# Kernel tuning notes

Measured on AMD Instinct MI355X. Metric: run time of the kernel, lower is better.

## Reference

```python
import jax, jax.numpy as jnp
import numpy as np

T, B, P, H = 4096, 16, 512, 512
DT_MIN, DT_MAX = 1e-3, 0.1


def setup_inputs() -> dict:
    key = jax.random.key(0)
    k_in, k_b, k_dt = jax.random.split(key, 3)
    inputs = jax.random.normal(k_in, (T, B, H), dtype=jnp.float32)
    # HiPPO-diag init: a_diag = -sqrt(2n+1)*sqrt(2n+3); log_neg_a = log(-a_diag)
    n = jnp.arange(P, dtype=jnp.float32)
    log_neg_a = jnp.log(jnp.sqrt(2 * n + 1) * jnp.sqrt(2 * n + 3))
    b = jax.random.normal(k_b, (P, H), dtype=jnp.float32) * 0.01
    log_dt = jax.random.uniform(k_dt, (P,), dtype=jnp.float32) * (
        np.float32(np.log(DT_MAX)) - np.float32(np.log(DT_MIN))
    ) + np.float32(np.log(DT_MIN))
    return {"inputs": inputs, "log_neg_a": log_neg_a, "b": b, "log_dt": log_dt}


def reference(inputs, log_neg_a, b, log_dt):
    # Discretization (matches torch module exactly, including extra dt factor)
    dt = jnp.exp(log_dt)                       # [P]
    a = -jnp.exp(log_neg_a)                    # [P]
    a_bar = jnp.exp(dt * a)                    # [P]
    b_bar = ((a_bar - 1.0) / a)[:, None] * b * dt[:, None]  # [P, H]

    # Precompute driving term for all timesteps: u_t @ b_bar.T -> [T, B, P]
    bu = jnp.einsum("tbh,ph->tbp", inputs, b_bar)

    batch = inputs.shape[1]
    z0 = jnp.zeros((batch, a_bar.shape[0]), dtype=inputs.dtype)

    def step(z, bu_t):
        z = a_bar[None, :] * z + bu_t
        return z, z

    _, zs = jax.lax.scan(step, z0, bu)  # [T, B, P]
    return zs
```

## Files before the change

### kernel.cpp

```cpp
#include <hip/hip_runtime.h>
#include <math.h>

#define T_DIM 4096
#define B_DIM 16
#define P_DIM 512
#define H_DIM 512
#define M_DIM (T_DIM * B_DIM)
#define BP (B_DIM * P_DIM)
#define BP4 (BP / 4)
#define P4 (P_DIM / 4)

#define KBYTES (H_DIM * 2)
#define BK 64

#define CLEN_F 8
#define CHUNKS_F (T_DIM / CLEN_F)
#define GROUP 16
#define NGROUPS (CHUNKS_F / GROUP)
#define CLEN_S 64
#define CHUNKS_S (T_DIM / CLEN_S)

#define SCALE_B 1048576.0f
#define INV_SCALE_B (1.0f / 1048576.0f)

typedef _Float16 f16x8 __attribute__((ext_vector_type(8)));
typedef float f32x4 __attribute__((ext_vector_type(4)));

__device__ __forceinline__ void gload16(const void* g, void* l) {
    __builtin_amdgcn_global_load_lds(
        (const __attribute__((address_space(1))) void*)(uintptr_t)g,
        (__attribute__((address_space(3))) void*)(uint32_t)(uintptr_t)l,
        16, 0, 0);
}

__global__ __launch_bounds__(256) void precompute_kernel(
    const float* __restrict__ log_neg_a,
    const float* __restrict__ b,
    const float* __restrict__ log_dt,
    float* __restrict__ b_bar,
    _Float16* __restrict__ b_bar16,
    float* __restrict__ a_bar,
    float* __restrict__ aL8,
    float* __restrict__ aL128,
    float* __restrict__ aL64,
    float* __restrict__ aL8pow,
    int write16) {
    int idx = blockIdx.x * blockDim.x + threadIdx.x;
    if (idx >= P_DIM * H_DIM) return;
    int p = idx >> 9;
    float dt = expf(log_dt[p]);
    float a  = -expf(log_neg_a[p]);
    float x  = dt * a;
    float scale = (expm1f(x) / a) * dt;
    float bb = scale * b[idx];
    b_bar[idx] = bb;
    if (write16) b_bar16[idx] = (_Float16)(bb * SCALE_B);
    if ((idx & (H_DIM - 1)) == 0) {
        a_bar[p] = expf(x);
        float l8 = expf(x * 8.0f);
        aL8[p]   = l8;
        aL128[p] = expf(x * 128.0f);
        aL64[p]  = expf(x * 64.0f);
        float pw = 1.0f;
        for (int j = 0; j < GROUP; ++j) {
            aL8pow[j * P_DIM + p] = pw;
            pw *= l8;
        }
    }
}

__global__ __launch_bounds__(256) void convert_a_kernel(
    const float4* __restrict__ in, f16x8* __restrict__ out) {
    int t = blockIdx.x * blockDim.x + threadIdx.x;
    float4 v0 = in[(size_t)t * 2];
    float4 v1 = in[(size_t)t * 2 + 1];
    f16x8 o;
    o[0] = (_Float16)v0.x; o[1] = (_Float16)v0.y;
    o[2] = (_Float16)v0.z; o[3] = (_Float16)v0.w;
    o[4] = (_Float16)v1.x; o[5] = (_Float16)v1.y;
    o[6] = (_Float16)v1.z; o[7] = (_Float16)v1.w;
    out[t] = o;
}

__global__ __launch_bounds__(256) void gemm16_scan_kernel(
    const char* __restrict__ A16,
    const char* __restrict__ B16,
    const float* __restrict__ a_bar,
    float* __restrict__ Cout,
    float* __restrict__ carry) {
    __shared__ char As[128 * BK * 2];
    __shared__ char Bs[128 * BK * 2];

    const int tid  = threadIdx.x;
    const int lane = tid & 63;
    const int wid  = tid >> 6;
    const int rowBase = blockIdx.y * 128;
    const int colBase = blockIdx.x * 128;

    const int srow = tid >> 3;
    const int scol = ((tid & 7) << 4) ^ ((srow & 7) << 4);
    const char* gA = A16 + (size_t)(rowBase + srow) * KBYTES + scol;
    const char* gB = B16 + (size_t)(colBase + srow) * KBYTES + scol;

    f32x4 acc[4][4];
#pragma unroll
    for (int m2 = 0; m2 < 4; ++m2)
#pragma unroll
        for (int n2 = 0; n2 < 4; ++n2)
            acc[m2][n2] = (f32x4){0.f, 0.f, 0.f, 0.f};

    const int wr = wid >> 1;
    const int wc = wid & 1;

    for (int kt = 0; kt < H_DIM / BK; ++kt) {
#pragma unroll
        for (int i = 0; i < 4; ++i) {
            gload16(gA + (size_t)i * 32 * KBYTES, As + (i * 256 + wid * 64) * 16);
            gload16(gB + (size_t)i * 32 * KBYTES, Bs + (i * 256 + wid * 64) * 16);
        }
        gA += BK * 2;
        gB += BK * 2;
        __syncthreads();

#pragma unroll
        for (int kk = 0; kk < 2; ++kk) {
            const int kbyte = kk * 64 + ((lane >> 4) << 4);
            f16x8 af[4], bf[4];
#pragma unroll
            for (int m2 = 0; m2 < 4; ++m2) {
                int row = wr * 64 + m2 * 16 + (lane & 15);
                af[m2] = *(const f16x8*)(As + row * 128 + (kbyte ^ ((row & 7) << 4)));
            }
#pragma unroll
            for (int n2 = 0; n2 < 4; ++n2) {
                int col = wc * 64 + n2 * 16 + (lane & 15);
                bf[n2] = *(const f16x8*)(Bs + col * 128 + (kbyte ^ ((col & 7) << 4)));
            }
#pragma unroll
            for (int m2 = 0; m2 < 4; ++m2)
#pragma unroll
                for (int n2 = 0; n2 < 4; ++n2)
                    acc[m2][n2] = __builtin_amdgcn_mfma_f32_16x16x32_f16(
                        af[m2], bf[n2], acc[m2][n2], 0, 0, 0);
        }
        __syncthreads();
    }

    float* lds_z = (float*)As;
    const int pl = wc * 64 + (lane & 15);

    float ab[4];
#pragma unroll
    for (int n2 = 0; n2 < 4; ++n2) ab[n2] = a_bar[colBase + pl + n2 * 16];

    if (wr == 0) {
#pragma unroll
        for (int n2 = 0; n2 < 4; ++n2)
#pragma unroll
            for (int r = 0; r < 4; ++r) {
                float z = 0.f;
#pragma unroll
                for (int m2 = 0; m2 < 4; ++m2) {
                    z = fmaf(ab[n2], z, acc[m2][n2][r]);
                    acc[m2][n2][r] = z;
                }
                lds_z[((lane >> 4) * 4 + r) * 128 + pl + n2 * 16] = z;
            }
    }
    __syncthreads();
    if (wr == 1) {
#pragma unroll
        for (int n2 = 0; n2 < 4; ++n2)
#pragma unroll
            for (int r = 0; r < 4; ++r) {
                float z = lds_z[((lane >> 4) * 4 + r) * 128 + pl + n2 * 16];
#pragma unroll
                for (int m2 = 0; m2 < 4; ++m2) {
                    z = fmaf(ab[n2], z, acc[m2][n2][r]);
                    acc[m2][n2][r] = z;
                }
                int b = (lane >> 4) * 4 + r;
                carry[(size_t)blockIdx.y * BP + b * P_DIM + colBase + pl + n2 * 16] =
                    z * INV_SCALE_B;
            }
    }

#pragma unroll
    for (int m2 = 0; m2 < 4; ++m2) {
#pragma unroll
        for (int r = 0; r < 4; ++r) {
            size_t row = (size_t)(rowBase + wr * 64 + m2 * 16 + (lane >> 4) * 4 + r);
            float* po = Cout + row * P_DIM + colBase + wc * 64 + (lane & 15);
#pragma unroll
            for (int n2 = 0; n2 < 4; ++n2)
                po[n2 * 16] = acc[m2][n2][r] * INV_SCALE_B;
        }
    }
}

__global__ __launch_bounds__(256) void group_scan_kernel(
    const float4* __restrict__ carry,
    const float4* __restrict__ aL8_4,
    float4* __restrict__ y,
    float4* __restrict__ G) {
    int tid = blockIdx.x * blockDim.x + threadIdx.x;
    int bp4 = tid & (BP4 - 1);
    int g = tid >> 11;
    float4 ab = aL8_4[bp4 & (P4 - 1)];
    float4 z = make_float4(0.f, 0.f, 0.f, 0.f);
#pragma unroll
    for (int j = 0; j < GROUP; ++j) {
        size_t c = (size_t)(g * GROUP + j) * BP4 + bp4;
        y[c] = z;
        float4 v = carry[c];
        z.x = fmaf(ab.x, z.x, v.x);
        z.y = fmaf(ab.y, z.y, v.y);
        z.z = fmaf(ab.z, z.z, v.z);
        z.w = fmaf(ab.w, z.w, v.w);
    }
    G[(size_t)g * BP4 + bp4] = z;
}

__global__ __launch_bounds__(256) void gcarry_scan_kernel(
    const float* __restrict__ G,
    const float* __restrict__ aL128,
    float* __restrict__ gz) {
    int bp = blockIdx.x * blockDim.x + threadIdx.x;
    float aL = aL128[bp & (P_DIM - 1)];
    float z = 0.f;
#pragma unroll
    for (int g = 0; g < NGROUPS; ++g) {
        gz[g * BP + bp] = z;
        z = fmaf(aL, z, G[g * BP + bp]);
    }
}

__global__ __launch_bounds__(256) void fixup8_kernel(
    float4* __restrict__ zio,
    const float4* __restrict__ a_bar4,
    const float4* __restrict__ y,
    const float4* __restrict__ gz,
    const float4* __restrict__ aL8pow4) {
    int tid = blockIdx.x * blockDim.x + threadIdx.x;
    int bp4 = tid & (BP4 - 1);
    int c = (tid >> 11) + 1;
    int p4 = bp4 & (P4 - 1);
    int g = c >> 4;
    int j = c & (GROUP - 1);
    float4 ab = a_bar4[p4];
    float4 pw = aL8pow4[j * P4 + p4];
    float4 yy = y[(size_t)c * BP4 + bp4];
    float4 gzz = gz[(size_t)g * BP4 + bp4];
    float4 zin;
    zin.x = fmaf(pw.x, gzz.x, yy.x);
    zin.y = fmaf(pw.y, gzz.y, yy.y);
    zin.z = fmaf(pw.z, gzz.z, yy.z);
    zin.w = fmaf(pw.w, gzz.w, yy.w);
    float4 f = ab;
    size_t base = (size_t)c * CLEN_F * BP4 + bp4;
#pragma unroll
    for (int i = 0; i < CLEN_F; ++i) {
        size_t off = base + (size_t)i * BP4;
        float4 v = zio[off];
        v.x = fmaf(f.x, zin.x, v.x);
        v.y = fmaf(f.y, zin.y, v.y);
        v.z = fmaf(f.z, zin.z, v.z);
        v.w = fmaf(f.w, zin.w, v.w);
        zio[off] = v;
        f.x *= ab.x;
        f.y *= ab.y;
        f.z *= ab.z;
        f.w *= ab.w;
    }
}

#define BM 128
#define BN 128
#define BKF 16
__global__ __launch_bounds__(256) void gemm_kernel(
    const float* __restrict__ A,
    const float* __restrict__ Bm,
    float* __restrict__ Cout) {
    __shared__ float As[BM][BKF + 1];
    __shared__ float Bs[BN][BKF + 4];
    const int K = H_DIM;
    const int N = P_DIM;
    int tid = threadIdx.x;
    int tx = tid & 15;
    int ty = tid >> 4;
    int rowBase = blockIdx.y * BM;
    int colBase = blockIdx.x * BN;
    float acc[8][8];
#pragma unroll
    for (int i = 0; i < 8; ++i)
#pragma unroll
        for (int j = 0; j < 8; ++j) acc[i][j] = 0.f;
    for (int kt = 0; kt < K; kt += BKF) {
#pragma unroll
        for (int l = 0; l < 2; ++l) {
            int fl = tid * 2 + l;
            int row = fl >> 2;
            int kq = fl & 3;
            float4 av = *reinterpret_cast<const float4*>(
                &A[(size_t)(rowBase + row) * K + kt + kq * 4]);
            As[row][kq * 4 + 0] = av.x;
            As[row][kq * 4 + 1] = av.y;
            As[row][kq * 4 + 2] = av.z;
            As[row][kq * 4 + 3] = av.w;
            float4 bv = *reinterpret_cast<const float4*>(
                &Bm[(size_t)(colBase + row) * K + kt + kq * 4]);
            *reinterpret_cast<float4*>(&Bs[row][kq * 4]) = bv;
        }
        __syncthreads();
#pragma unroll
        for (int k = 0; k < BKF; ++k) {
            float af[8], bf[8];
#pragma unroll
            for (int i = 0; i < 8; ++i) af[i] = As[ty * 8 + i][k];
#pragma unroll
            for (int j = 0; j < 8; ++j) bf[j] = Bs[tx + 16 * j][k];
#pragma unroll
            for (int i = 0; i < 8; ++i)
#pragma unroll
                for (int j = 0; j < 8; ++j)
                    acc[i][j] = fmaf(af[i], bf[j], acc[i][j]);
        }
        __syncthreads();
    }
#pragma unroll
    for (int i = 0; i < 8; ++i) {
        size_t r = (size_t)(rowBase + ty * 8 + i);
#pragma unroll
        for (int j = 0; j < 8; ++j)
            Cout[r * N + colBase + tx + 16 * j] = acc[i][j];
    }
}

__global__ __launch_bounds__(256) void scan_local_kernel(
    float4* __restrict__ zio,
    const float4* __restrict__ a_bar4,
    float4* __restrict__ carry) {
    int tid = blockIdx.x * blockDim.x + threadIdx.x;
    int bp4 = tid & (BP4 - 1);
    int c = tid >> 11;
    float4 ab = a_bar4[bp4 & (P4 - 1)];
    size_t base = (size_t)c * CLEN_S * BP4 + bp4;
    float4 z = make_float4(0.f, 0.f, 0.f, 0.f);
    for (int i = 0; i < CLEN_S; ++i) {
        size_t off = base + (size_t)i * BP4;
        float4 v = zio[off];
        z.x = fmaf(ab.x, z.x, v.x);
        z.y = fmaf(ab.y, z.y, v.y);
        z.z = fmaf(ab.z, z.z, v.z);
        z.w = fmaf(ab.w, z.w, v.w);
        zio[off] = z;
    }
    carry[tid] = z;
}

__global__ __launch_bounds__(256) void carry_scan_kernel(
    const float4* __restrict__ carry,
    const float4* __restrict__ aL4,
    float4* __restrict__ z_in,
    int nchunks) {
    int bp4 = blockIdx.x * blockDim.x + threadIdx.x;
    float4 aL = aL4[bp4 & (P4 - 1)];
    float4 z = make_float4(0.f, 0.f, 0.f, 0.f);
    for (int c = 0; c < nchunks; ++c) {
        z_in[(size_t)c * BP4 + bp4] = z;
        float4 v = carry[(size_t)c * BP4 + bp4];
        z.x = fmaf(aL.x, z.x, v.x);
        z.y = fmaf(aL.y, z.y, v.y);
        z.z = fmaf(aL.z, z.z, v.z);
        z.w = fmaf(aL.w, z.w, v.w);
    }
}

__global__ __launch_bounds__(256) void fixup_kernel(
    float4* __restrict__ zio,
    const float4* __restrict__ a_bar4,
    const float4* __restrict__ z_in,
    int clen) {
    int tid = blockIdx.x * blockDim.x + threadIdx.x;
    int bp4 = tid & (BP4 - 1);
    int c = (tid >> 11) + 1;
    float4 ab = a_bar4[bp4 & (P4 - 1)];
    float4 zin = z_in[(size_t)c * BP4 + bp4];
    float4 f = ab;
    size_t base = (size_t)c * clen * BP4 + bp4;
    for (int i = 0; i < clen; ++i) {
        size_t off = base + (size_t)i * BP4;
        float4 v = zio[off];
        v.x = fmaf(f.x, zin.x, v.x);
        v.y = fmaf(f.y, zin.y, v.y);
        v.z = fmaf(f.z, zin.z, v.z);
        v.w = fmaf(f.w, zin.w, v.w);
        zio[off] = v;
        f.x *= ab.x;
        f.y *= ab.y;
        f.z *= ab.z;
        f.w *= ab.w;
    }
}

extern "C" void kernel_launch(void* const* d_in, const int* in_sizes, int n_in,
                              void* d_out, int out_size, void* d_ws, size_t ws_size,
                              hipStream_t stream) {
    const float* inputs    = (const float*)d_in[0];
    const float* log_neg_a = (const float*)d_in[1];
    const float* b         = (const float*)d_in[2];
    const float* log_dt    = (const float*)d_in[3];
    float* out = (float*)d_out;
    float* ws  = (float*)d_ws;

    float* b_bar   = ws;
    float* a_bar   = b_bar + P_DIM * H_DIM;
    float* aL8     = a_bar + P_DIM;
    float* aL128   = aL8 + P_DIM;
    float* aL64    = aL128 + P_DIM;
    float* aL8pow  = aL64 + P_DIM;
    float* carry   = aL8pow + GROUP * P_DIM;
    float* y       = carry + (size_t)CHUNKS_F * BP;
    float* G       = y + (size_t)CHUNKS_F * BP;
    float* gz      = G + (size_t)NGROUPS * BP;
    float* tail    = gz + (size_t)NGROUPS * BP;
    _Float16* b_bar16 = (_Float16*)tail;
    _Float16* A16     = b_bar16 + P_DIM * H_DIM;

    size_t ws_need = (size_t)((char*)(A16 + (size_t)M_DIM * H_DIM) - (char*)ws);
    int fast = (ws_size >= ws_need);

    precompute_kernel<<<(P_DIM * H_DIM) / 256, 256, 0, stream>>>(
        log_neg_a, b, log_dt, b_bar, b_bar16, a_bar, aL8, aL128, aL64, aL8pow, fast);

    if (fast) {
        convert_a_kernel<<<(M_DIM * H_DIM / 8) / 256, 256, 0, stream>>>(
            (const float4*)inputs, (f16x8*)A16);

        dim3 ggrid(P_DIM / 128, M_DIM / 128);
        gemm16_scan_kernel<<<ggrid, 256, 0, stream>>>(
            (const char*)A16, (const char*)b_bar16, a_bar, out, carry);

        group_scan_kernel<<<(NGROUPS * BP4) / 256, 256, 0, stream>>>(
            (const float4*)carry, (const float4*)aL8, (float4*)y, (float4*)G);

        gcarry_scan_kernel<<<BP / 256, 256, 0, stream>>>(G, aL128, gz);

        fixup8_kernel<<<((CHUNKS_F - 1) * BP4) / 256, 256, 0, stream>>>(
            (float4*)out, (const float4*)a_bar, (const float4*)y,
            (const float4*)gz, (const float4*)aL8pow);
    } else {
        dim3 ggrid(P_DIM / BN, M_DIM / BM);
        gemm_kernel<<<ggrid, 256, 0, stream>>>(inputs, b_bar, out);

        scan_local_kernel<<<(CHUNKS_S * BP4) / 256, 256, 0, stream>>>(
            (float4*)out, (const float4*)a_bar, (float4*)carry);

        carry_scan_kernel<<<BP4 / 256, 256, 0, stream>>>(
            (const float4*)carry, (const float4*)aL64, (float4*)y, CHUNKS_S);

        fixup_kernel<<<((CHUNKS_S - 1) * BP4) / 256, 256, 0, stream>>>(
            (float4*)out, (const float4*)a_bar, (const float4*)y, CLEN_S);
    }
}
```

Measured before the change: 161.3 us.

## Fuse fp32-to-fp16 input conversion into GEMM tile load

Removes the separate kernel that converted the fp32 inputs into an fp16 copy in workspace. The GEMM now loads fp32 A tiles straight into LDS with a swizzled layout and converts them to fp16 in registers before the MFMA. This avoids writing the 64 MB fp16 copy and reading it back. In exchange each GEMM block reads twice as many A bytes from global memory (the A input is read once per P-tile, of which there are four), uses double the LDS for A, and spends extra conversion instructions inside the inner loop.

```diff
diff --git a/kernel.cpp b/kernel.cpp
--- a/kernel.cpp
+++ b/kernel.cpp
@@ -10,7 +10,6 @@
 #define BP4 (BP / 4)
 #define P4 (P_DIM / 4)
 
-#define KBYTES (H_DIM * 2)
 #define BK 64
 
 #define CLEN_F 8
@@ -69,26 +68,13 @@
     }
 }
 
-__global__ __launch_bounds__(256) void convert_a_kernel(
-    const float4* __restrict__ in, f16x8* __restrict__ out) {
-    int t = blockIdx.x * blockDim.x + threadIdx.x;
-    float4 v0 = in[(size_t)t * 2];
-    float4 v1 = in[(size_t)t * 2 + 1];
-    f16x8 o;
-    o[0] = (_Float16)v0.x; o[1] = (_Float16)v0.y;
-    o[2] = (_Float16)v0.z; o[3] = (_Float16)v0.w;
-    o[4] = (_Float16)v1.x; o[5] = (_Float16)v1.y;
-    o[6] = (_Float16)v1.z; o[7] = (_Float16)v1.w;
-    out[t] = o;
-}
-
-__global__ __launch_bounds__(256) void gemm16_scan_kernel(
-    const char* __restrict__ A16,
+__global__ __launch_bounds__(256) void gemm_f32a_scan_kernel(
+    const float* __restrict__ A,
     const char* __restrict__ B16,
     const float* __restrict__ a_bar,
     float* __restrict__ Cout,
     float* __restrict__ carry) {
-    __shared__ char As[128 * BK * 2];
+    __shared__ char As[128 * BK * 4];
     __shared__ char Bs[128 * BK * 2];
 
     const int tid  = threadIdx.x;
@@ -97,10 +83,13 @@
     const int rowBase = blockIdx.y * 128;
     const int colBase = blockIdx.x * 128;
 
+    const int arow = tid >> 4;
+    const int acolb = (((tid & 15) ^ ((tid >> 4) & 7)) << 4);
+    const char* gA = (const char*)(A + (size_t)(rowBase + arow) * H_DIM) + acolb;
+
     const int srow = tid >> 3;
-    const int scol = ((tid & 7) << 4) ^ ((srow & 7) << 4);
-    const char* gA = A16 + (size_t)(rowBase + srow) * KBYTES + scol;
-    const char* gB = B16 + (size_t)(colBase + srow) * KBYTES + scol;
+    const int scolb = ((tid & 7) << 4) ^ ((srow & 7) << 4);
+    const char* gB = B16 + (size_t)(colBase + srow) * (H_DIM * 2) + scolb;
 
     f32x4 acc[4][4];
 #pragma unroll
@@ -114,27 +103,37 @@
 
     for (int kt = 0; kt < H_DIM / BK; ++kt) {
 #pragma unroll
-        for (int i = 0; i < 4; ++i) {
-            gload16(gA + (size_t)i * 32 * KBYTES, As + (i * 256 + wid * 64) * 16);
-            gload16(gB + (size_t)i * 32 * KBYTES, Bs + (i * 256 + wid * 64) * 16);
-        }
-        gA += BK * 2;
+        for (int i = 0; i < 8; ++i)
+            gload16(gA + (size_t)i * 16 * (H_DIM * 4), As + (i * 256 + wid * 64) * 16);
+#pragma unroll
+        for (int i = 0; i < 4; ++i)
+            gload16(gB + (size_t)i * 32 * (H_DIM * 2), Bs + (i * 256 + wid * 64) * 16);
+        gA += BK * 4;
         gB += BK * 2;
         __syncthreads();
 
 #pragma unroll
         for (int kk = 0; kk < 2; ++kk) {
-            const int kbyte = kk * 64 + ((lane >> 4) << 4);
+            const int ch0 = kk * 8 + ((lane >> 4) << 1);
+            const int kbyteB = kk * 64 + ((lane >> 4) << 4);
             f16x8 af[4], bf[4];
 #pragma unroll
             for (int m2 = 0; m2 < 4; ++m2) {
                 int row = wr * 64 + m2 * 16 + (lane & 15);
-                af[m2] = *(const f16x8*)(As + row * 128 + (kbyte ^ ((row & 7) << 4)));
+                int sw = (row & 7);
+                float4 a0 = *(const float4*)(As + row * 256 + ((ch0 ^ sw) << 4));
+                float4 a1 = *(const float4*)(As + row * 256 + (((ch0 + 1) ^ sw) << 4));
+                f16x8 v;
+                v[0] = (_Float16)a0.x; v[1] = (_Float16)a0.y;
+                v[2] = (_Float16)a0.z; v[3] = (_Float16)a0.w;
+                v[4] = (_Float16)a1.x; v[5] = (_Float16)a1.y;
+                v[6] = (_Float16)a1.z; v[7] = (_Float16)a1.w;
+                af[m2] = v;
             }
 #pragma unroll
             for (int n2 = 0; n2 < 4; ++n2) {
                 int col = wc * 64 + n2 * 16 + (lane & 15);
-                bf[n2] = *(const f16x8*)(Bs + col * 128 + (kbyte ^ ((col & 7) << 4)));
+                bf[n2] = *(const f16x8*)(Bs + col * 128 + (kbyteB ^ ((col & 7) << 4)));
             }
 #pragma unroll
             for (int m2 = 0; m2 < 4; ++m2)
@@ -425,21 +424,17 @@
     float* gz      = G + (size_t)NGROUPS * BP;
     float* tail    = gz + (size_t)NGROUPS * BP;
     _Float16* b_bar16 = (_Float16*)tail;
-    _Float16* A16     = b_bar16 + P_DIM * H_DIM;
-
-    size_t ws_need = (size_t)((char*)(A16 + (size_t)M_DIM * H_DIM) - (char*)ws);
+
+    size_t ws_need = (size_t)((char*)(b_bar16 + (size_t)P_DIM * H_DIM) - (char*)ws);
     int fast = (ws_size >= ws_need);
 
     precompute_kernel<<<(P_DIM * H_DIM) / 256, 256, 0, stream>>>(
         log_neg_a, b, log_dt, b_bar, b_bar16, a_bar, aL8, aL128, aL64, aL8pow, fast);
 
     if (fast) {
-        convert_a_kernel<<<(M_DIM * H_DIM / 8) / 256, 256, 0, stream>>>(
-            (const float4*)inputs, (f16x8*)A16);
-
         dim3 ggrid(P_DIM / 128, M_DIM / 128);
-        gemm16_scan_kernel<<<ggrid, 256, 0, stream>>>(
-            (const char*)A16, (const char*)b_bar16, a_bar, out, carry);
+        gemm_f32a_scan_kernel<<<ggrid, 256, 0, stream>>>(
+            inputs, (const char*)b_bar16, a_bar, out, carry);
 
         group_scan_kernel<<<(NGROUPS * BP4) / 256, 256, 0, stream>>>(
             (const float4*)carry, (const float4*)aL8, (float4*)y, (float4*)G);
```

After: 170.4 us. +5.6%, slower.
